# Kernel optimization log

Measured on AMD Instinct MI355X. Metric: run time of the kernel, lower is better.

## Reference

```python
import jax, jax.numpy as jnp
import numpy as np

N = 50000      # num nodes
E = 400000     # num edges
D = 384        # input_dim
H = 4          # heads
C = 128        # hidden_dim per head
HC = H * C     # 512


def setup_inputs() -> dict:
    key = jax.random.key(0)
    ks = jax.random.split(key, 32)
    w = lambda k, shape: jax.random.normal(k, shape, jnp.float32) * 0.05
    inp = {
        "x": jax.random.normal(ks[0], (N, D), jnp.float32),
        "edge_index": jax.random.randint(ks[1], (2, E), 0, N, dtype=jnp.int32),
    }
    dims = [(D, HC), (HC, HC)]  # layer0 in=384, layer1 in=512
    i = 2
    for l, (din, dout) in enumerate(dims):
        for nm in ["q", "k", "v", "s"]:  # query/key/value/skip linears
            inp[f"{nm}{l}_w"] = w(ks[i], (dout, din)); i += 1
            inp[f"{nm}{l}_b"] = jnp.zeros((dout,), jnp.float32)
    inp["out_w"] = w(ks[i], (D, HC))
    inp["out_b"] = jnp.zeros((D,), jnp.float32)
    return inp


def _transformer_conv(x, src, dst, Wq, bq, Wk, bk, Wv, bv, Ws, bs):
    # PyG TransformerConv, concat=True, root_weight=True, no edge features.
    n = x.shape[0]
    q = (x @ Wq.T + bq).reshape(n, H, C)
    k = (x @ Wk.T + bk).reshape(n, H, C)
    v = (x @ Wv.T + bv).reshape(n, H, C)
    # per-edge attention logits [E, H]; target = dst, source = src
    alpha = (q[dst] * k[src]).sum(-1) / jnp.sqrt(jnp.float32(C))
    m = jax.ops.segment_max(alpha, dst, num_segments=n)
    m = jnp.where(jnp.isfinite(m), m, 0.0)  # nodes with no in-edges
    e = jnp.exp(alpha - m[dst])
    denom = jax.ops.segment_sum(e, dst, num_segments=n)
    a = e / (denom[dst] + 1e-16)             # segment softmax [E, H]
    msg = v[src] * a[:, :, None]             # [E, H, C]
    agg = jax.ops.segment_sum(msg, dst, num_segments=n).reshape(n, HC)
    return agg + x @ Ws.T + bs               # + root/skip connection


def reference(x, edge_index,
              q0_w, q0_b, k0_w, k0_b, v0_w, v0_b, s0_w, s0_b,
              q1_w, q1_b, k1_w, k1_b, v1_w, v1_b, s1_w, s1_b,
              out_w, out_b):
    src, dst = edge_index[0], edge_index[1]
    h = _transformer_conv(x, src, dst, q0_w, q0_b, k0_w, k0_b, v0_w, v0_b, s0_w, s0_b)
    h = jax.nn.relu(h)
    h = _transformer_conv(h, src, dst, q1_w, q1_b, k1_w, k1_b, v1_w, v1_b, s1_w, s1_b)
    h = jax.nn.relu(h)
    return h @ out_w.T + out_b  # [N, D]
```

## Files before the change

kernel.cpp:

```cpp
#include <hip/hip_runtime.h>
#include <hip/hip_bf16.h>

#define NN 50000
#define NE 400000
#define DD 384
#define HC 512

typedef unsigned int u32;
typedef unsigned short u16;
typedef __attribute__((ext_vector_type(8))) short bf16x8;
typedef __attribute__((ext_vector_type(4))) float f32x4;

#define AS1 __attribute__((address_space(1)))
#define AS3 __attribute__((address_space(3)))

__device__ __forceinline__ float bflo(u32 u){ return __uint_as_float(u << 16); }
__device__ __forceinline__ float bfhi(u32 u){ return __uint_as_float(u & 0xFFFF0000u); }
__device__ __forceinline__ u16 f2bf(float f){
    u32 u = __float_as_uint(f);
    return (u16)((u + 0x7FFFu + ((u >> 16) & 1u)) >> 16);
}
__device__ __forceinline__ u32 pack2(float a, float b){
    return (u32)f2bf(a) | ((u32)f2bf(b) << 16);
}

template<int K>
__global__ __launch_bounds__(512)
void gemm_ws(const u16* __restrict__ Ab, const u16* __restrict__ Wb,
             const float* __restrict__ bias,
             u16* __restrict__ oQ, u16* __restrict__ oK,
             u16* __restrict__ oV, u16* __restrict__ oS)
{
    constexpr int NKC  = K / 32;
    constexpr int NPAN = (NN + 127) / 128;
    __shared__ char smW[NKC * 8192];
    __shared__ char smA[2][16384];

    const int b   = blockIdx.x;
    const int xcd = b & 7;
    const int idx = b >> 3;
    const int ct  = idx & 15;
    const int rh  = idx >> 4;

    const int tid  = threadIdx.x;
    const int lane = tid & 63;
    const int w    = tid >> 6;
    const int wq   = w >> 1;
    const int wc   = w & 1;
    const int r16  = lane & 15;
    const int kq   = lane >> 4;

    {
        const u16* Wrow0 = Wb + (size_t)ct * 128 * K;
        const int row = tid >> 2, pc = tid & 3;
        const int lc  = pc ^ (row & 3);
        #pragma unroll
        for (int kt = 0; kt < NKC; ++kt) {
            uint4 v = *(const uint4*)(Wrow0 + (size_t)row * K + kt * 32 + lc * 8);
            *(uint4*)(smW + kt * 8192 + tid * 16) = v;
        }
    }
    asm volatile("s_waitcnt lgkmcnt(0)" ::: "memory");
    __builtin_amdgcn_sched_barrier(0);

    int np = 0;
    while ((2 * np + rh) * 8 + xcd < NPAN) ++np;
    const int npair = (np + 1) / 2;
    const int total = npair * NKC;

    auto stageA = [&](int t2) {
        int jp2 = t2 / NKC, kc2 = t2 - jp2 * NKC;
        int p0 = (4 * jp2 + rh) * 8 + xcd;
        int p1 = (2 * jp2 + 1 < np) ? p0 + 16 : p0;
        const int row = tid >> 2, pc = tid & 3;
        const int lc  = pc ^ (row & 3);
        #pragma unroll
        for (int p = 0; p < 2; ++p) {
            int pan = p ? p1 : p0;
            int gr = pan * 128 + row; if (gr >= NN) gr = NN - 1;
            __builtin_amdgcn_global_load_lds(
                (const AS1 u32*)(Ab + (size_t)gr * K + kc2 * 32 + lc * 8),
                (AS3 u32*)(smA[t2 & 1] + (p * 512 + tid) * 16), 16, 0, 0);
        }
    };

    stageA(0);
    if (total > 1) stageA(1);

    f32x4 acc[2][2][4] = {};

    const int qsel = ct >> 2;
    u16* outp = (qsel == 0) ? oQ : (qsel == 1) ? oK : (qsel == 2) ? oV : oS;
    const int cb = (ct & 3) * 128 + wc * 64;
    float bv4[4];
    #pragma unroll
    for (int ni = 0; ni < 4; ++ni) bv4[ni] = bias[ct * 128 + wc * 64 + ni * 16 + r16];

    for (int t = 0; t < total; ++t) {
        if (t + 1 < total) { asm volatile("s_waitcnt vmcnt(2)" ::: "memory"); }
        else               { asm volatile("s_waitcnt vmcnt(0)" ::: "memory"); }
        __builtin_amdgcn_s_barrier();
        __builtin_amdgcn_sched_barrier(0);

        const int jp = t / NKC;
        const int kc = t - jp * NKC;
        const char* bufA = smA[t & 1];

        bf16x8 bv[4];
        #pragma unroll
        for (int ni = 0; ni < 4; ++ni) {
            int rowW = wc * 64 + ni * 16 + r16;
            bv[ni] = *(const bf16x8*)(smW + kc * 8192 + rowW * 64
                                      + ((kq ^ (rowW & 3)) << 4));
        }
        #pragma unroll
        for (int q = 0; q < 2; ++q) {
            #pragma unroll
            for (int mi = 0; mi < 2; ++mi) {
                int rowA = wq * 32 + mi * 16 + r16;
                bf16x8 av = *(const bf16x8*)(bufA + q * 8192 + rowA * 64
                                             + ((kq ^ (rowA & 3)) << 4));
                #pragma unroll
                for (int ni = 0; ni < 4; ++ni)
                    acc[q][mi][ni] = __builtin_amdgcn_mfma_f32_16x16x32_bf16(
                        av, bv[ni], acc[q][mi][ni], 0, 0, 0);
            }
        }

        __builtin_amdgcn_sched_barrier(0);
        __builtin_amdgcn_s_barrier();
        __builtin_amdgcn_sched_barrier(0);

        if (kc == NKC - 1) {
            int p0 = (4 * jp + rh) * 8 + xcd;
            int p1 = (2 * jp + 1 < np) ? p0 + 16 : p0;
            #pragma unroll
            for (int q = 0; q < 2; ++q) {
                int m0 = (q ? p1 : p0) * 128;
                #pragma unroll
                for (int ni = 0; ni < 4; ++ni) {
                    int col = cb + ni * 16 + r16;
                    float bb = bv4[ni];
                    #pragma unroll
                    for (int mi = 0; mi < 2; ++mi)
                        #pragma unroll
                        for (int r = 0; r < 4; ++r) {
                            int gr = m0 + wq * 32 + mi * 16 + kq * 4 + r;
                            if (gr < NN)
                                outp[(size_t)gr * 512 + col] = f2bf(acc[q][mi][ni][r] + bb);
                            acc[q][mi][ni][r] = 0.f;
                        }
                }
            }
        }
        if (t + 2 < total) stageA(t + 2);
    }
}

template<int K>
__global__ __launch_bounds__(256)
void gemm2ph(const u16* __restrict__ Ab, const u16* __restrict__ Wb,
             const float* __restrict__ bias, float* __restrict__ oF,
             int n, int Ototal, int NT)
{
    constexpr int NKT = K / 64;
    __shared__ char smA[2][16384];
    __shared__ char smB[2][16384];

    const int nb  = gridDim.x;
    const int bd  = blockIdx.x;
    const int q8  = nb >> 3, r8 = nb & 7;
    const int xcd = bd & 7, gg = bd >> 3;
    const int tt  = (xcd < r8 ? xcd * (q8 + 1) : r8 * (q8 + 1) + (xcd - r8) * q8) + gg;
    const int m0  = (tt / NT) * 128;
    const int o0  = (tt % NT) * 128;

    const int tid  = threadIdx.x;
    const int lane = tid & 63;
    const int w    = tid >> 6;
    const int wr   = w >> 1, wc = w & 1;
    const int r16  = lane & 15;
    const int kq   = lane >> 4;
    const int swz  = (r16 & 7) << 4;

    auto stage = [&](int bf, int kt) {
        #pragma unroll
        for (int p = 0; p < 4; ++p) {
            int ci = p * 256 + tid, row = ci >> 3, pc = ci & 7;
            int lc = pc ^ (row & 7);
            const u16* g = Wb + (size_t)(o0 + row) * K + kt * 64 + lc * 8;
            __builtin_amdgcn_global_load_lds((const AS1 u32*)g,
                                             (AS3 u32*)(smB[bf] + ci * 16), 16, 0, 0);
        }
        #pragma unroll
        for (int p = 0; p < 4; ++p) {
            int ci = p * 256 + tid, row = ci >> 3, pc = ci & 7;
            int lc = pc ^ (row & 7);
            int gr = m0 + row; if (gr >= n) gr = n - 1;
            const u16* g = Ab + (size_t)gr * K + kt * 64 + lc * 8;
            __builtin_amdgcn_global_load_lds((const AS1 u32*)g,
                                             (AS3 u32*)(smA[bf] + ci * 16), 16, 0, 0);
        }
    };

    f32x4 acc[4][4] = {};

    stage(0, 0);
    stage(1, 1);

    for (int kt = 0; kt < NKT; ++kt) {
        if (kt + 1 < NKT) { asm volatile("s_waitcnt vmcnt(8)" ::: "memory"); }
        else             { asm volatile("s_waitcnt vmcnt(0)" ::: "memory"); }
        __builtin_amdgcn_s_barrier();
        __builtin_amdgcn_sched_barrier(0);

        const char* pa = smA[kt & 1] + (wr * 64) * 128;
        const char* pb = smB[kt & 1] + (wc * 64) * 128;
        #pragma unroll
        for (int kk = 0; kk < 2; ++kk) {
            const int kb = kk * 64 + kq * 16;
            bf16x8 av[4], bv[4];
            #pragma unroll
            for (int i = 0; i < 4; ++i) {
                av[i] = *(const bf16x8*)(pa + (i * 16 + r16) * 128 + (kb ^ swz));
                bv[i] = *(const bf16x8*)(pb + (i * 16 + r16) * 128 + (kb ^ swz));
            }
            #pragma unroll
            for (int mi = 0; mi < 4; ++mi)
                #pragma unroll
                for (int ni = 0; ni < 4; ++ni)
                    acc[mi][ni] = __builtin_amdgcn_mfma_f32_16x16x32_bf16(
                        av[mi], bv[ni], acc[mi][ni], 0, 0, 0);
        }

        __builtin_amdgcn_sched_barrier(0);
        __builtin_amdgcn_s_barrier();
        __builtin_amdgcn_sched_barrier(0);
        if (kt + 2 < NKT) stage(kt & 1, kt + 2);
    }

    const int cbo = o0 + wc * 64;
    #pragma unroll
    for (int ni = 0; ni < 4; ++ni) {
        int col = cbo + ni * 16 + r16;
        float bb = bias[col];
        #pragma unroll
        for (int mi = 0; mi < 4; ++mi)
            #pragma unroll
            for (int r = 0; r < 4; ++r) {
                int gr = m0 + wr * 64 + mi * 16 + kq * 4 + r;
                if (gr < n) oF[(size_t)gr * Ototal + col] = acc[mi][ni][r] + bb;
            }
    }
}

#define XG  2400000
#define W0G 24576
#define W1G 32768
#define WOG 24576
#define CVT_TOTAL (XG + 4*W0G + 4*W1G + WOG)

__global__ __launch_bounds__(256)
void cvt_all(const float* __restrict__ x,
             const float* q0w, const float* k0w, const float* v0w, const float* s0w,
             const float* q1w, const float* k1w, const float* v1w, const float* s1w,
             const float* ow,
             u16* __restrict__ Xb, u16* __restrict__ Wc0,
             u16* __restrict__ Wc1, u16* __restrict__ WcO)
{
    int i = blockIdx.x * 256 + threadIdx.x;
    if (i >= CVT_TOTAL) return;
    const float* s; u16* d; int g;
    if (i < XG) { s = x; d = Xb; g = i; }
    else {
        int j = i - XG;
        if (j < 4 * W0G) {
            int q = j / W0G; g = j - q * W0G;
            s = (q == 0 ? q0w : q == 1 ? k0w : q == 2 ? v0w : s0w);
            d = Wc0 + (size_t)q * W0G * 8;
        } else if ((j -= 4 * W0G) < 4 * W1G) {
            int q = j / W1G; g = j - q * W1G;
            s = (q == 0 ? q1w : q == 1 ? k1w : q == 2 ? v1w : s1w);
            d = Wc1 + (size_t)q * W1G * 8;
        } else { j -= 4 * W1G; s = ow; d = WcO; g = j; }
    }
    float4 f0 = ((const float4*)s)[(size_t)g * 2];
    float4 f1 = ((const float4*)s)[(size_t)g * 2 + 1];
    uint4 o;
    o.x = pack2(f0.x, f0.y); o.y = pack2(f0.z, f0.w);
    o.z = pack2(f1.x, f1.y); o.w = pack2(f1.z, f1.w);
    ((uint4*)d)[g] = o;
}

__global__ __launch_bounds__(256)
void pack_bias(const float* q0, const float* k0, const float* v0, const float* s0,
               const float* q1, const float* k1, const float* v1, const float* s1,
               const float* ob, float* __restrict__ dst)
{
    int i = blockIdx.x * 256 + threadIdx.x;
    if (i >= 4480) return;
    float v;
    if (i < 2048) {
        int j = i & 511, q = i >> 9;
        v = (q == 0 ? q0 : q == 1 ? k0 : q == 2 ? v0 : s0)[j];
    } else if (i < 4096) {
        int j = i - 2048; int q = j >> 9; j &= 511;
        v = (q == 0 ? q1 : q == 1 ? k1 : q == 2 ? v1 : s1)[j];
    } else {
        v = ob[i - 4096];
    }
    dst[i] = v;
}

__global__ __launch_bounds__(256)
void zero_deg(int* __restrict__ deg)
{
    int i = blockIdx.x * 256 + threadIdx.x;
    if (i < NN) deg[i] = 0;
}

__global__ __launch_bounds__(256)
void hist_dst(const int* __restrict__ dst, int* __restrict__ deg)
{
    int e = blockIdx.x * 256 + threadIdx.x;
    if (e < NE) atomicAdd(&deg[dst[e]], 1);
}

__global__ __launch_bounds__(1024)
void scan_deg(const int* __restrict__ deg, int* __restrict__ rowptr,
              int* __restrict__ cursor)
{
    __shared__ int wsum[16];
    const int tid = threadIdx.x, lane = tid & 63, wid = tid >> 6;
    int carry = 0;
    for (int base = 0; base < NN; base += 1024) {
        int i = base + tid;
        int orig = (i < NN) ? deg[i] : 0;
        int v = orig;
        #pragma unroll
        for (int off = 1; off < 64; off <<= 1) {
            int t = __shfl_up(v, off, 64);
            if (lane >= off) v += t;
        }
        if (lane == 63) wsum[wid] = v;
        __syncthreads();
        if (wid == 0) {
            int s = (lane < 16) ? wsum[lane] : 0;
            #pragma unroll
            for (int off = 1; off < 16; off <<= 1) {
                int t = __shfl_up(s, off, 16);
                if ((lane & 15) >= off) s += t;
            }
            if (lane < 16) wsum[lane] = s;
        }
        __syncthreads();
        int woff  = (wid == 0) ? 0 : wsum[wid - 1];
        int total = wsum[15];
        int excl  = carry + woff + (v - orig);
        if (i < NN) { rowptr[i] = excl; cursor[i] = excl; }
        carry += total;
        __syncthreads();
    }
    if (tid == 0) rowptr[NN] = NE;
}

__global__ __launch_bounds__(256)
void scatter_edges(const int* __restrict__ src, const int* __restrict__ dst,
                   int* __restrict__ cursor, int* __restrict__ esrc_ord)
{
    int e = blockIdx.x * 256 + threadIdx.x;
    if (e >= NE) return;
    int pos = atomicAdd(&cursor[dst[e]], 1);
    esrc_ord[pos] = src[e];
}

__global__ __launch_bounds__(256)
void node_attn(const u16* __restrict__ Qb, const u16* __restrict__ Kb,
               const u16* __restrict__ Vb, const int* __restrict__ rowptr,
               const int* __restrict__ esrc, const u16* __restrict__ skipb,
               u16* __restrict__ outb)
{
    int d = blockIdx.x * 4 + (threadIdx.x >> 6);
    if (d >= NN) return;
    int lane = threadIdx.x & 63;

    uint4 qv = *((const uint4*)(Qb + (size_t)d * HC) + lane);
    float q[8] = { bflo(qv.x), bfhi(qv.x), bflo(qv.y), bfhi(qv.y),
                   bflo(qv.z), bfhi(qv.z), bflo(qv.w), bfhi(qv.w) };

    int beg = rowptr[d], end = rowptr[d + 1];
    float m = -INFINITY, den = 0.f;
    float acc[8] = {};

    for (int i = beg; i < end; ++i) {
        int s = esrc[i];
        uint4 kv = *((const uint4*)(Kb + (size_t)s * HC) + lane);
        float sum = q[0] * bflo(kv.x) + q[1] * bfhi(kv.x)
                  + q[2] * bflo(kv.y) + q[3] * bfhi(kv.y)
                  + q[4] * bflo(kv.z) + q[5] * bfhi(kv.z)
                  + q[6] * bflo(kv.w) + q[7] * bfhi(kv.w);
        #pragma unroll
        for (int off = 1; off < 16; off <<= 1) sum += __shfl_xor(sum, off, 64);
        float alpha = sum * 0.08838834764831845f;

        float mnew  = fmaxf(m, alpha);
        float scale = __expf(m - mnew);
        float p     = __expf(alpha - mnew);
        den = den * scale + p;

        uint4 vv = *((const uint4*)(Vb + (size_t)s * HC) + lane);
        acc[0] = acc[0] * scale + p * bflo(vv.x);
        acc[1] = acc[1] * scale + p * bfhi(vv.x);
        acc[2] = acc[2] * scale + p * bflo(vv.y);
        acc[3] = acc[3] * scale + p * bfhi(vv.y);
        acc[4] = acc[4] * scale + p * bflo(vv.z);
        acc[5] = acc[5] * scale + p * bfhi(vv.z);
        acc[6] = acc[6] * scale + p * bflo(vv.w);
        acc[7] = acc[7] * scale + p * bfhi(vv.w);
        m = mnew;
    }

    float inv = 1.f / (den + 1e-16f);
    size_t base = (size_t)d * HC + lane * 8;
    uint4 sv = *((const uint4*)(skipb + base));
    float sk[8] = { bflo(sv.x), bfhi(sv.x), bflo(sv.y), bfhi(sv.y),
                    bflo(sv.z), bfhi(sv.z), bflo(sv.w), bfhi(sv.w) };
    uint4 o;
    o.x = pack2(fmaxf(acc[0] * inv + sk[0], 0.f), fmaxf(acc[1] * inv + sk[1], 0.f));
    o.y = pack2(fmaxf(acc[2] * inv + sk[2], 0.f), fmaxf(acc[3] * inv + sk[3], 0.f));
    o.z = pack2(fmaxf(acc[4] * inv + sk[4], 0.f), fmaxf(acc[5] * inv + sk[5], 0.f));
    o.w = pack2(fmaxf(acc[6] * inv + sk[6], 0.f), fmaxf(acc[7] * inv + sk[7], 0.f));
    *(uint4*)(outb + base) = o;
}

extern "C" void kernel_launch(void* const* d_in, const int* in_sizes, int n_in,
                              void* d_out, int out_size, void* d_ws, size_t ws_size,
                              hipStream_t stream)
{
    const float* x   = (const float*)d_in[0];
    const int* ei    = (const int*)d_in[1];
    const int* esrc  = ei;
    const int* edst  = ei + NE;
    const float* q0w = (const float*)d_in[2];  const float* q0b = (const float*)d_in[3];
    const float* k0w = (const float*)d_in[4];  const float* k0b = (const float*)d_in[5];
    const float* v0w = (const float*)d_in[6];  const float* v0b = (const float*)d_in[7];
    const float* s0w = (const float*)d_in[8];  const float* s0b = (const float*)d_in[9];
    const float* q1w = (const float*)d_in[10]; const float* q1b = (const float*)d_in[11];
    const float* k1w = (const float*)d_in[12]; const float* k1b = (const float*)d_in[13];
    const float* v1w = (const float*)d_in[14]; const float* v1b = (const float*)d_in[15];
    const float* s1w = (const float*)d_in[16]; const float* s1b = (const float*)d_in[17];
    const float* ow  = (const float*)d_in[18]; const float* obs = (const float*)d_in[19];

    char* p = (char*)d_ws;
    auto take = [&](size_t bytes) { void* r = (void*)p; p += (bytes + 255) & ~(size_t)255; return r; };
    u16*   Qb     = (u16*)take((size_t)NN * HC * 2);
    u16*   Vb     = (u16*)take((size_t)NN * HC * 2);
    u16*   Hb     = (u16*)take((size_t)NN * HC * 2);
    u16*   Sb     = (u16*)take((size_t)NN * HC * 2);
    u16*   Xb     = (u16*)take((size_t)NN * DD * 2);
    u16*   Wc0    = (u16*)take((size_t)2048 * DD * 2);
    u16*   Wc1    = (u16*)take((size_t)2048 * HC * 2);
    u16*   WcO    = (u16*)take((size_t)DD * HC * 2);
    float* barena = (float*)take(4480 * 4);

    char* dob = (char*)d_out;
    u16* Kb       = (u16*)dob;
    int* deg      = (int*)(dob + 51200000);
    int* rowptr   = (int*)(dob + 51400192);
    int* cursor   = (int*)(dob + 51600384);
    int* esrc_ord = (int*)(dob + 51800576);

    dim3 blk(256);
    int gN   = (NN + 255) / 256;
    int gE   = (NE + 255) / 256;
    int gnod = (NN + 3) / 4;
    const int NPAN = (NN + 127) / 128;
    int go = NPAN * 3;

    pack_bias<<<(4480 + 255) / 256, blk, 0, stream>>>(q0b, k0b, v0b, s0b,
                                                      q1b, k1b, v1b, s1b, obs, barena);
    cvt_all<<<(CVT_TOTAL + 255) / 256, blk, 0, stream>>>(x,
        q0w, k0w, v0w, s0w, q1w, k1w, v1w, s1w, ow, Xb, Wc0, Wc1, WcO);

    zero_deg      <<<gN, blk, 0, stream>>>(deg);
    hist_dst      <<<gE, blk, 0, stream>>>(edst, deg);
    scan_deg      <<<1, 1024, 0, stream>>>(deg, rowptr, cursor);
    scatter_edges <<<gE, blk, 0, stream>>>(esrc, edst, cursor, esrc_ord);

    gemm_ws<DD><<<256, 512, 0, stream>>>(Xb, Wc0, barena, Qb, Kb, Vb, Sb);
    node_attn<<<gnod, blk, 0, stream>>>(Qb, Kb, Vb, rowptr, esrc_ord, Sb, Hb);

    gemm_ws<HC><<<256, 512, 0, stream>>>(Hb, Wc1, barena + 2048, Qb, Kb, Vb, Sb);
    node_attn<<<gnod, blk, 0, stream>>>(Qb, Kb, Vb, rowptr, esrc_ord, Sb, Hb);

    gemm2ph<HC><<<go, blk, 0, stream>>>(Hb, WcO, barena + 4096,
                                        (float*)d_out, NN, 384, 3);
}
```

Before: 736.3 us.

## Restructure weight-stationary GEMM to 256 threads, K-64 tiles, vectorized transposed stores

The weight-stationary projection GEMM now runs 256-thread blocks that process one 128-row panel per step with 64-wide K tiles. The resident weight tile is loaded asynchronously through global_load_lds with an XOR swizzle, and the vmcnt waits are retuned to match. In both GEMMs the MFMA operands are swapped so each lane holds four consecutive output columns, which allows packed uint2 bf16 stores and float4 fp32 stores in place of scalar stores. The aim is fewer, wider global writes and more MFMA work per LDS load, at the cost of fewer waves per block and a larger LDS weight buffer.

```diff
diff --git a/kernel.cpp b/kernel.cpp
--- a/kernel.cpp
+++ b/kernel.cpp
@@ -25,15 +25,16 @@
 }
 
 template<int K>
-__global__ __launch_bounds__(512)
+__global__ __launch_bounds__(256)
 void gemm_ws(const u16* __restrict__ Ab, const u16* __restrict__ Wb,
              const float* __restrict__ bias,
              u16* __restrict__ oQ, u16* __restrict__ oK,
              u16* __restrict__ oV, u16* __restrict__ oS)
 {
-    constexpr int NKC  = K / 32;
+    constexpr int NKT  = K / 64;
+    constexpr int WCH  = K / 8;
     constexpr int NPAN = (NN + 127) / 128;
-    __shared__ char smW[NKC * 8192];
+    __shared__ char smW[128 * K * 2];
     __shared__ char smA[2][16384];
 
     const int b   = blockIdx.x;
@@ -45,111 +46,100 @@
     const int tid  = threadIdx.x;
     const int lane = tid & 63;
     const int w    = tid >> 6;
-    const int wq   = w >> 1;
-    const int wc   = w & 1;
+    const int wr   = w >> 1, wc = w & 1;
     const int r16  = lane & 15;
     const int kq   = lane >> 4;
 
     {
-        const u16* Wrow0 = Wb + (size_t)ct * 128 * K;
-        const int row = tid >> 2, pc = tid & 3;
-        const int lc  = pc ^ (row & 3);
-        #pragma unroll
-        for (int kt = 0; kt < NKC; ++kt) {
-            uint4 v = *(const uint4*)(Wrow0 + (size_t)row * K + kt * 32 + lc * 8);
-            *(uint4*)(smW + kt * 8192 + tid * 16) = v;
-        }
-    }
-    asm volatile("s_waitcnt lgkmcnt(0)" ::: "memory");
-    __builtin_amdgcn_sched_barrier(0);
+        const u16* W0 = Wb + (size_t)ct * 128 * K;
+        #pragma unroll
+        for (int p = 0; p < (128 * WCH) / 256; ++p) {
+            int ci = p * 256 + tid;
+            int row = ci / WCH, pc = ci % WCH;
+            int lc = (pc & ~7) | ((pc ^ row) & 7);
+            __builtin_amdgcn_global_load_lds((const AS1 u32*)(W0 + (size_t)row * K + lc * 8),
+                                             (AS3 u32*)(smW + (size_t)ci * 16), 16, 0, 0);
+        }
+    }
 
     int np = 0;
     while ((2 * np + rh) * 8 + xcd < NPAN) ++np;
-    const int npair = (np + 1) / 2;
-    const int total = npair * NKC;
-
-    auto stageA = [&](int t2) {
-        int jp2 = t2 / NKC, kc2 = t2 - jp2 * NKC;
-        int p0 = (4 * jp2 + rh) * 8 + xcd;
-        int p1 = (2 * jp2 + 1 < np) ? p0 + 16 : p0;
-        const int row = tid >> 2, pc = tid & 3;
-        const int lc  = pc ^ (row & 3);
-        #pragma unroll
-        for (int p = 0; p < 2; ++p) {
-            int pan = p ? p1 : p0;
-            int gr = pan * 128 + row; if (gr >= NN) gr = NN - 1;
-            __builtin_amdgcn_global_load_lds(
-                (const AS1 u32*)(Ab + (size_t)gr * K + kc2 * 32 + lc * 8),
-                (AS3 u32*)(smA[t2 & 1] + (p * 512 + tid) * 16), 16, 0, 0);
+    const int total = np * NKT;
+
+    auto stageA = [&](int t) {
+        int jp = t / NKT, kc = t - jp * NKT;
+        int m0 = ((2 * jp + rh) * 8 + xcd) * 128;
+        #pragma unroll
+        for (int p = 0; p < 4; ++p) {
+            int ci = p * 256 + tid;
+            int row = ci >> 3, pc = ci & 7;
+            int lc = pc ^ (row & 7);
+            int gr = m0 + row; if (gr >= NN) gr = NN - 1;
+            __builtin_amdgcn_global_load_lds((const AS1 u32*)(Ab + (size_t)gr * K + kc * 64 + lc * 8),
+                                             (AS3 u32*)(smA[t & 1] + ci * 16), 16, 0, 0);
         }
     };
 
     stageA(0);
     if (total > 1) stageA(1);
 
-    f32x4 acc[2][2][4] = {};
+    f32x4 acc[4][4] = {};
 
     const int qsel = ct >> 2;
     u16* outp = (qsel == 0) ? oQ : (qsel == 1) ? oK : (qsel == 2) ? oV : oS;
     const int cb = (ct & 3) * 128 + wc * 64;
-    float bv4[4];
+    float bb[4][4];
     #pragma unroll
-    for (int ni = 0; ni < 4; ++ni) bv4[ni] = bias[ct * 128 + wc * 64 + ni * 16 + r16];
+    for (int ni = 0; ni < 4; ++ni)
+        #pragma unroll
+        for (int r = 0; r < 4; ++r)
+            bb[ni][r] = bias[ct * 128 + wc * 64 + ni * 16 + kq * 4 + r];
 
     for (int t = 0; t < total; ++t) {
-        if (t + 1 < total) { asm volatile("s_waitcnt vmcnt(2)" ::: "memory"); }
-        else               { asm volatile("s_waitcnt vmcnt(0)" ::: "memory"); }
+        const int jp = t / NKT, kc = t - jp * NKT;
+        if (t + 1 >= total)                { asm volatile("s_waitcnt vmcnt(0)"  ::: "memory"); }
+        else if (kc == 0 && t > 0)         { asm volatile("s_waitcnt vmcnt(20)" ::: "memory"); }
+        else                               { asm volatile("s_waitcnt vmcnt(4)"  ::: "memory"); }
         __builtin_amdgcn_s_barrier();
         __builtin_amdgcn_sched_barrier(0);
 
-        const int jp = t / NKC;
-        const int kc = t - jp * NKC;
-        const char* bufA = smA[t & 1];
-
-        bf16x8 bv[4];
-        #pragma unroll
-        for (int ni = 0; ni < 4; ++ni) {
-            int rowW = wc * 64 + ni * 16 + r16;
-            bv[ni] = *(const bf16x8*)(smW + kc * 8192 + rowW * 64
-                                      + ((kq ^ (rowW & 3)) << 4));
-        }
-        #pragma unroll
-        for (int q = 0; q < 2; ++q) {
-            #pragma unroll
-            for (int mi = 0; mi < 2; ++mi) {
-                int rowA = wq * 32 + mi * 16 + r16;
-                bf16x8 av = *(const bf16x8*)(bufA + q * 8192 + rowA * 64
-                                             + ((kq ^ (rowA & 3)) << 4));
+        const char* pa = smA[t & 1] + (wr * 64) * 128;
+        #pragma unroll
+        for (int kk = 0; kk < 2; ++kk) {
+            const int slot = (((kk << 2) + kq) ^ (r16 & 7)) << 4;
+            bf16x8 av[4], bv[4];
+            #pragma unroll
+            for (int i = 0; i < 4; ++i) {
+                av[i] = *(const bf16x8*)(pa + (i * 16 + r16) * 128 + slot);
+                int rw = wc * 64 + i * 16 + r16;
+                bv[i] = *(const bf16x8*)(smW + (size_t)rw * (K * 2) + kc * 128 + slot);
+            }
+            #pragma unroll
+            for (int mi = 0; mi < 4; ++mi)
                 #pragma unroll
                 for (int ni = 0; ni < 4; ++ni)
-                    acc[q][mi][ni] = __builtin_amdgcn_mfma_f32_16x16x32_bf16(
-                        av, bv[ni], acc[q][mi][ni], 0, 0, 0);
-            }
+                    acc[mi][ni] = __builtin_amdgcn_mfma_f32_16x16x32_bf16(
+                        bv[ni], av[mi], acc[mi][ni], 0, 0, 0);
         }
 
         __builtin_amdgcn_sched_barrier(0);
         __builtin_amdgcn_s_barrier();
         __builtin_amdgcn_sched_barrier(0);
 
-        if (kc == NKC - 1) {
-            int p0 = (4 * jp + rh) * 8 + xcd;
-            int p1 = (2 * jp + 1 < np) ? p0 + 16 : p0;
-            #pragma unroll
-            for (int q = 0; q < 2; ++q) {
-                int m0 = (q ? p1 : p0) * 128;
+        if (kc == NKT - 1) {
+            int m0 = ((2 * jp + rh) * 8 + xcd) * 128;
+            #pragma unroll
+            for (int mi = 0; mi < 4; ++mi) {
+                int gr = m0 + wr * 64 + mi * 16 + r16;
+                bool ok = gr < NN;
                 #pragma unroll
                 for (int ni = 0; ni < 4; ++ni) {
-                    int col = cb + ni * 16 + r16;
-                    float bb = bv4[ni];
+                    uint2 o;
+                    o.x = pack2(acc[mi][ni][0] + bb[ni][0], acc[mi][ni][1] + bb[ni][1]);
+                    o.y = pack2(acc[mi][ni][2] + bb[ni][2], acc[mi][ni][3] + bb[ni][3]);
+                    if (ok) *(uint2*)(outp + (size_t)gr * 512 + cb + ni * 16 + kq * 4) = o;
                     #pragma unroll
-                    for (int mi = 0; mi < 2; ++mi)
-                        #pragma unroll
-                        for (int r = 0; r < 4; ++r) {
-                            int gr = m0 + wq * 32 + mi * 16 + kq * 4 + r;
-                            if (gr < NN)
-                                outp[(size_t)gr * 512 + col] = f2bf(acc[q][mi][ni][r] + bb);
-                            acc[q][mi][ni][r] = 0.f;
-                        }
+                    for (int r = 0; r < 4; ++r) acc[mi][ni][r] = 0.f;
                 }
             }
         }
@@ -181,7 +171,6 @@
     const int wr   = w >> 1, wc = w & 1;
     const int r16  = lane & 15;
     const int kq   = lane >> 4;
-    const int swz  = (r16 & 7) << 4;
 
     auto stage = [&](int bf, int kt) {
         #pragma unroll
@@ -218,19 +207,19 @@
         const char* pb = smB[kt & 1] + (wc * 64) * 128;
         #pragma unroll
         for (int kk = 0; kk < 2; ++kk) {
-            const int kb = kk * 64 + kq * 16;
+            const int slot = (((kk << 2) + kq) ^ (r16 & 7)) << 4;
             bf16x8 av[4], bv[4];
             #pragma unroll
             for (int i = 0; i < 4; ++i) {
-                av[i] = *(const bf16x8*)(pa + (i * 16 + r16) * 128 + (kb ^ swz));
-                bv[i] = *(const bf16x8*)(pb + (i * 16 + r16) * 128 + (kb ^ swz));
+                av[i] = *(const bf16x8*)(pa + (i * 16 + r16) * 128 + kk * 0 + slot + 0);
+                bv[i] = *(const bf16x8*)(pb + (i * 16 + r16) * 128 + slot);
             }
             #pragma unroll
             for (int mi = 0; mi < 4; ++mi)
                 #pragma unroll
                 for (int ni = 0; ni < 4; ++ni)
                     acc[mi][ni] = __builtin_amdgcn_mfma_f32_16x16x32_bf16(
-                        av[mi], bv[ni], acc[mi][ni], 0, 0, 0);
+                        bv[ni], av[mi], acc[mi][ni], 0, 0, 0);
         }
 
         __builtin_amdgcn_sched_barrier(0);
@@ -239,18 +228,19 @@
         if (kt + 2 < NKT) stage(kt & 1, kt + 2);
     }
 
-    const int cbo = o0 + wc * 64;
     #pragma unroll
-    for (int ni = 0; ni < 4; ++ni) {
-        int col = cbo + ni * 16 + r16;
-        float bb = bias[col];
-        #pragma unroll
-        for (int mi = 0; mi < 4; ++mi)
-            #pragma unroll
-            for (int r = 0; r < 4; ++r) {
-                int gr = m0 + wr * 64 + mi * 16 + kq * 4 + r;
-                if (gr < n) oF[(size_t)gr * Ototal + col] = acc[mi][ni][r] + bb;
-            }
+    for (int mi = 0; mi < 4; ++mi) {
+        int gr = m0 + wr * 64 + mi * 16 + r16;
+        if (gr >= n) continue;
+        #pragma unroll
+        for (int ni = 0; ni < 4; ++ni) {
+            int col = o0 + wc * 64 + ni * 16 + kq * 4;
+            float4 o = make_float4(acc[mi][ni][0] + bias[col],
+                                   acc[mi][ni][1] + bias[col + 1],
+                                   acc[mi][ni][2] + bias[col + 2],
+                                   acc[mi][ni][3] + bias[col + 3]);
+            *(float4*)(oF + (size_t)gr * Ototal + col) = o;
+        }
     }
 }
 
@@ -487,10 +477,10 @@
     scan_deg      <<<1, 1024, 0, stream>>>(deg, rowptr, cursor);
     scatter_edges <<<gE, blk, 0, stream>>>(esrc, edst, cursor, esrc_ord);
 
-    gemm_ws<DD><<<256, 512, 0, stream>>>(Xb, Wc0, barena, Qb, Kb, Vb, Sb);
+    gemm_ws<DD><<<256, 256, 0, stream>>>(Xb, Wc0, barena, Qb, Kb, Vb, Sb);
     node_attn<<<gnod, blk, 0, stream>>>(Qb, Kb, Vb, rowptr, esrc_ord, Sb, Hb);
 
-    gemm_ws<HC><<<256, 512, 0, stream>>>(Hb, Wc1, barena + 2048, Qb, Kb, Vb, Sb);
+    gemm_ws<HC><<<256, 256, 0, stream>>>(Hb, Wc1, barena + 2048, Qb, Kb, Vb, Sb);
     node_attn<<<gnod, blk, 0, stream>>>(Qb, Kb, Vb, rowptr, esrc_ord, Sb, Hb);
 
     gemm2ph<HC><<<go, blk, 0, stream>>>(Hb, WcO, barena + 4096,
```

Result: slower. 811.9 us (+10.3%).
